# Kernel tuning notes

Measured on AMD Instinct MI355X. Metric: run time of the kernel, lower is better.

## Reference

```python
import jax, jax.numpy as jnp
import numpy as np

D_MODEL = 1024
NUM_BLOCKS = 4

def setup_inputs() -> dict:
    key = jax.random.key(0)
    k1, k2 = jax.random.split(key)
    x = jax.random.normal(k1, (8, 4096, D_MODEL), dtype=jnp.float32)
    # Linear(d_model, d_model) params, torch-style fan_in init scale
    W = jax.random.normal(k2, (D_MODEL, D_MODEL), dtype=jnp.float32) * (1.0 / np.sqrt(D_MODEL))
    b = jnp.zeros((D_MODEL,), dtype=jnp.float32)
    return {"x": x, "W": W, "b": b, "num_blocks": NUM_BLOCKS}

def reference(x, W, b, num_blocks):
    # x: [B, L, D]; split L into num_blocks blocks; SE-style gating per block.
    B, L, D = x.shape
    bs = L // num_blocks
    xb = x.reshape(B, num_blocks, bs, D)          # [B, nb, bs, D]
    pooled = jnp.mean(xb, axis=2)                 # avg-pool over block length -> [B, nb, D]
    gate = jax.nn.sigmoid(jnp.einsum('bnd,ed->bne', pooled, W) + b)  # Linear + sigmoid
    out = xb * gate[:, :, None, :]                # broadcast over block length
    return out.reshape(B, L, D)
```

## Files before the change

kernel.cpp:

```cpp
#include <hip/hip_runtime.h>

#define B      8
#define L      4096
#define D      1024
#define NB     4
#define BS     (L / NB)
#define BN     (B * NB)
#define SPLITS 64
#define ROWS_PER (BS / SPLITS)

__global__ void pool_partial(const float* __restrict__ x, float* __restrict__ partial) {
    int gid = blockIdx.x;
    int s   = gid & (SPLITS - 1);
    int bn  = gid >> 6;
    int t   = threadIdx.x;

    const float4* xb = (const float4*)(x + (size_t)bn * BS * D + (size_t)s * ROWS_PER * D);
    float4 acc = make_float4(0.f, 0.f, 0.f, 0.f);
    #pragma unroll
    for (int r = 0; r < ROWS_PER; ++r) {
        float4 v = xb[(size_t)r * (D / 4) + t];
        acc.x += v.x; acc.y += v.y; acc.z += v.z; acc.w += v.w;
    }
    float4* p = (float4*)(partial + ((size_t)bn * SPLITS + s) * D);
    p[t] = acc;
}

__global__ void gate_kernel(const float* __restrict__ partial, const float* __restrict__ W,
                            const float* __restrict__ bias, float* __restrict__ gate) {
    __shared__ float4 pool_s[D / 4];

    int blk = blockIdx.x;
    int bn  = blk >> 3;
    int et  = blk & 7;
    int t   = threadIdx.x;

    const float4* p = (const float4*)(partial + (size_t)bn * SPLITS * D);
    float4 acc = make_float4(0.f, 0.f, 0.f, 0.f);
    #pragma unroll
    for (int s = 0; s < SPLITS; ++s) {
        float4 v = p[(size_t)s * (D / 4) + t];
        acc.x += v.x; acc.y += v.y; acc.z += v.z; acc.w += v.w;
    }
    const float inv = 1.0f / (float)BS;
    pool_s[t] = make_float4(acc.x * inv, acc.y * inv, acc.z * inv, acc.w * inv);
    __syncthreads();

    int wv   = t >> 6;
    int lane = t & 63;

    float4 pf[4];
    #pragma unroll
    for (int c = 0; c < 4; ++c) pf[c] = pool_s[c * 64 + lane];

    int ebase = et * 128 + wv * 32;
    for (int i = 0; i < 32; i += 4) {
        float s0 = 0.f, s1 = 0.f, s2 = 0.f, s3 = 0.f;
        #pragma unroll
        for (int c = 0; c < 4; ++c) {
            float4 w0 = ((const float4*)(W + (size_t)(ebase + i + 0) * D))[c * 64 + lane];
            float4 w1 = ((const float4*)(W + (size_t)(ebase + i + 1) * D))[c * 64 + lane];
            float4 w2 = ((const float4*)(W + (size_t)(ebase + i + 2) * D))[c * 64 + lane];
            float4 w3 = ((const float4*)(W + (size_t)(ebase + i + 3) * D))[c * 64 + lane];
            float4 pp = pf[c];
            s0 += w0.x * pp.x + w0.y * pp.y + w0.z * pp.z + w0.w * pp.w;
            s1 += w1.x * pp.x + w1.y * pp.y + w1.z * pp.z + w1.w * pp.w;
            s2 += w2.x * pp.x + w2.y * pp.y + w2.z * pp.z + w2.w * pp.w;
            s3 += w3.x * pp.x + w3.y * pp.y + w3.z * pp.z + w3.w * pp.w;
        }
        #pragma unroll
        for (int off = 32; off; off >>= 1) {
            s0 += __shfl_down(s0, off);
            s1 += __shfl_down(s1, off);
            s2 += __shfl_down(s2, off);
            s3 += __shfl_down(s3, off);
        }
        if (lane == 0) {
            int e = ebase + i;
            gate[(size_t)bn * D + e + 0] = 1.0f / (1.0f + __expf(-(s0 + bias[e + 0])));
            gate[(size_t)bn * D + e + 1] = 1.0f / (1.0f + __expf(-(s1 + bias[e + 1])));
            gate[(size_t)bn * D + e + 2] = 1.0f / (1.0f + __expf(-(s2 + bias[e + 2])));
            gate[(size_t)bn * D + e + 3] = 1.0f / (1.0f + __expf(-(s3 + bias[e + 3])));
        }
    }
}

__global__ void apply_gate(const float* __restrict__ x, const float* __restrict__ gate,
                           float* __restrict__ out) {
    const size_t total4 = (size_t)B * L * D / 4;
    const float4* x4 = (const float4*)x;
    const float4* g4 = (const float4*)gate;
    float4* o4 = (float4*)out;

    for (size_t f = (size_t)blockIdx.x * blockDim.x + threadIdx.x; f < total4;
         f += (size_t)gridDim.x * blockDim.x) {
        size_t row = f >> 8;
        int bn = (int)((row >> 12) * NB + ((row >> 10) & (NB - 1)));
        float4 g = g4[(size_t)bn * (D / 4) + (f & 255)];
        float4 v = x4[f];
        o4[f] = make_float4(v.x * g.x, v.y * g.y, v.z * g.z, v.w * g.w);
    }
}

extern "C" void kernel_launch(void* const* d_in, const int* in_sizes, int n_in,
                              void* d_out, int out_size, void* d_ws, size_t ws_size,
                              hipStream_t stream) {
    const float* x    = (const float*)d_in[0];
    const float* W    = (const float*)d_in[1];
    const float* bias = (const float*)d_in[2];
    float* out        = (float*)d_out;

    float* partial = (float*)d_ws;
    float* gate    = partial + (size_t)BN * SPLITS * D;

    hipLaunchKernelGGL(pool_partial, dim3(BN * SPLITS), dim3(256), 0, stream, x, partial);
    hipLaunchKernelGGL(gate_kernel,  dim3(BN * 8),      dim3(256), 0, stream, partial, W, bias, gate);
    hipLaunchKernelGGL(apply_gate,   dim3(4096),        dim3(256), 0, stream, x, gate, out);
}
```

Before: 288.8 us.

## Split pooled reduction into its own kernel, widen gate grid, block-structured apply with nontemporal stores

Moves the reduction of partial sums into a separate pool_reduce kernel, so the gate kernel no longer repeats that 64-way reduction in each of its blocks. The gate kernel now runs 32 blocks per batch-block with 8 outputs per wave, giving more parallelism over W. apply_gate switches from a grid-stride loop to one block per 4 rows, loading the gate vector once per block and writing output with nontemporal stores. This adds a kernel launch and an extra small global round trip for the pooled vector.

After: 270.7 us, median of 2. -6.3%, faster.

```diff
diff --git a/kernel.cpp b/kernel.cpp
--- a/kernel.cpp
+++ b/kernel.cpp
@@ -8,6 +8,8 @@
 #define BN     (B * NB)
 #define SPLITS 64
 #define ROWS_PER (BS / SPLITS)
+
+typedef __attribute__((ext_vector_type(4))) float f32x4;
 
 __global__ void pool_partial(const float* __restrict__ x, float* __restrict__ partial) {
     int gid = blockIdx.x;
@@ -22,46 +24,48 @@
         float4 v = xb[(size_t)r * (D / 4) + t];
         acc.x += v.x; acc.y += v.y; acc.z += v.z; acc.w += v.w;
     }
-    float4* p = (float4*)(partial + ((size_t)bn * SPLITS + s) * D);
-    p[t] = acc;
+    ((float4*)(partial + ((size_t)bn * SPLITS + s) * D))[t] = acc;
 }
 
-__global__ void gate_kernel(const float* __restrict__ partial, const float* __restrict__ W,
-                            const float* __restrict__ bias, float* __restrict__ gate) {
-    __shared__ float4 pool_s[D / 4];
-
-    int blk = blockIdx.x;
-    int bn  = blk >> 3;
-    int et  = blk & 7;
-    int t   = threadIdx.x;
-
+__global__ void pool_reduce(const float* __restrict__ partial, float* __restrict__ pooled) {
+    int bn = blockIdx.x;
+    int t  = threadIdx.x;
     const float4* p = (const float4*)(partial + (size_t)bn * SPLITS * D);
     float4 acc = make_float4(0.f, 0.f, 0.f, 0.f);
-    #pragma unroll
+    #pragma unroll 8
     for (int s = 0; s < SPLITS; ++s) {
         float4 v = p[(size_t)s * (D / 4) + t];
         acc.x += v.x; acc.y += v.y; acc.z += v.z; acc.w += v.w;
     }
     const float inv = 1.0f / (float)BS;
-    pool_s[t] = make_float4(acc.x * inv, acc.y * inv, acc.z * inv, acc.w * inv);
-    __syncthreads();
+    ((float4*)(pooled + (size_t)bn * D))[t] =
+        make_float4(acc.x * inv, acc.y * inv, acc.z * inv, acc.w * inv);
+}
 
+__global__ void gate_kernel(const float* __restrict__ pooled, const float* __restrict__ W,
+                            const float* __restrict__ bias, float* __restrict__ gate) {
+    int blk  = blockIdx.x;
+    int bn   = blk >> 5;
+    int et   = blk & 31;
+    int t    = threadIdx.x;
     int wv   = t >> 6;
     int lane = t & 63;
 
+    const float4* p4 = (const float4*)(pooled + (size_t)bn * D);
     float4 pf[4];
     #pragma unroll
-    for (int c = 0; c < 4; ++c) pf[c] = pool_s[c * 64 + lane];
+    for (int c = 0; c < 4; ++c) pf[c] = p4[c * 64 + lane];
 
-    int ebase = et * 128 + wv * 32;
-    for (int i = 0; i < 32; i += 4) {
+    const int ewv = et * 32 + wv * 8;
+    #pragma unroll
+    for (int i = 0; i < 8; i += 4) {
         float s0 = 0.f, s1 = 0.f, s2 = 0.f, s3 = 0.f;
         #pragma unroll
         for (int c = 0; c < 4; ++c) {
-            float4 w0 = ((const float4*)(W + (size_t)(ebase + i + 0) * D))[c * 64 + lane];
-            float4 w1 = ((const float4*)(W + (size_t)(ebase + i + 1) * D))[c * 64 + lane];
-            float4 w2 = ((const float4*)(W + (size_t)(ebase + i + 2) * D))[c * 64 + lane];
-            float4 w3 = ((const float4*)(W + (size_t)(ebase + i + 3) * D))[c * 64 + lane];
+            float4 w0 = ((const float4*)(W + (size_t)(ewv + i + 0) * D))[c * 64 + lane];
+            float4 w1 = ((const float4*)(W + (size_t)(ewv + i + 1) * D))[c * 64 + lane];
+            float4 w2 = ((const float4*)(W + (size_t)(ewv + i + 2) * D))[c * 64 + lane];
+            float4 w3 = ((const float4*)(W + (size_t)(ewv + i + 3) * D))[c * 64 + lane];
             float4 pp = pf[c];
             s0 += w0.x * pp.x + w0.y * pp.y + w0.z * pp.z + w0.w * pp.w;
             s1 += w1.x * pp.x + w1.y * pp.y + w1.z * pp.z + w1.w * pp.w;
@@ -76,7 +80,7 @@
             s3 += __shfl_down(s3, off);
         }
         if (lane == 0) {
-            int e = ebase + i;
+            int e = ewv + i;
             gate[(size_t)bn * D + e + 0] = 1.0f / (1.0f + __expf(-(s0 + bias[e + 0])));
             gate[(size_t)bn * D + e + 1] = 1.0f / (1.0f + __expf(-(s1 + bias[e + 1])));
             gate[(size_t)bn * D + e + 2] = 1.0f / (1.0f + __expf(-(s2 + bias[e + 2])));
@@ -87,18 +91,19 @@
 
 __global__ void apply_gate(const float* __restrict__ x, const float* __restrict__ gate,
                            float* __restrict__ out) {
-    const size_t total4 = (size_t)B * L * D / 4;
-    const float4* x4 = (const float4*)x;
-    const float4* g4 = (const float4*)gate;
-    float4* o4 = (float4*)out;
+    int blk = blockIdx.x;
+    int bn  = blk >> 8;
+    int s   = blk & 255;
+    int t   = threadIdx.x;
 
-    for (size_t f = (size_t)blockIdx.x * blockDim.x + threadIdx.x; f < total4;
-         f += (size_t)gridDim.x * blockDim.x) {
-        size_t row = f >> 8;
-        int bn = (int)((row >> 12) * NB + ((row >> 10) & (NB - 1)));
-        float4 g = g4[(size_t)bn * (D / 4) + (f & 255)];
-        float4 v = x4[f];
-        o4[f] = make_float4(v.x * g.x, v.y * g.y, v.z * g.z, v.w * g.w);
+    float4 gv = ((const float4*)(gate + (size_t)bn * D))[t];
+    const float4* xb = (const float4*)(x + ((size_t)bn * BS + (size_t)s * 4) * D);
+    float4* ob = (float4*)(out + ((size_t)bn * BS + (size_t)s * 4) * D);
+    #pragma unroll
+    for (int r = 0; r < 4; ++r) {
+        float4 v = xb[(size_t)r * (D / 4) + t];
+        float4 o = make_float4(v.x * gv.x, v.y * gv.y, v.z * gv.z, v.w * gv.w);
+        __builtin_nontemporal_store(*(const f32x4*)&o, (f32x4*)&ob[(size_t)r * (D / 4) + t]);
     }
 }
 
@@ -111,9 +116,11 @@
     float* out        = (float*)d_out;
 
     float* partial = (float*)d_ws;
-    float* gate    = partial + (size_t)BN * SPLITS * D;
+    float* pooled  = partial + (size_t)BN * SPLITS * D;
+    float* gate    = pooled + (size_t)BN * D;
 
     hipLaunchKernelGGL(pool_partial, dim3(BN * SPLITS), dim3(256), 0, stream, x, partial);
-    hipLaunchKernelGGL(gate_kernel,  dim3(BN * 8),      dim3(256), 0, stream, partial, W, bias, gate);
-    hipLaunchKernelGGL(apply_gate,   dim3(4096),        dim3(256), 0, stream, x, gate, out);
+    hipLaunchKernelGGL(pool_reduce,  dim3(BN),          dim3(256), 0, stream, partial, pooled);
+    hipLaunchKernelGGL(gate_kernel,  dim3(BN * 32),     dim3(256), 0, stream, pooled, W, bias, gate);
+    hipLaunchKernelGGL(apply_gate,   dim3(8192),        dim3(256), 0, stream, x, gate, out);
 }
```
